# Kernel tuning notes

Measured on AMD Instinct MI355X. Metric: run time of the kernel, lower is better.

The kernel has to match this reference:

```python
import jax, jax.numpy as jnp
import numpy as np

LN_EPS = 1e-5


def setup_inputs() -> dict:
    key = jax.random.key(0)
    ks = jax.random.split(key, 12)
    B, T, U, H, V = 4, 512, 128, 512, 41
    src = jax.random.normal(ks[0], (B, T, H), dtype=jnp.float32)
    tgt = jax.random.normal(ks[1], (B, U, H), dtype=jnp.float32)
    src_len = jax.random.randint(ks[2], (B,), 1, T + 1, dtype=jnp.int32)
    tgt_len = jax.random.randint(ks[3], (B,), 1, U + 1, dtype=jnp.int32)
    s = 1.0 / np.sqrt(H)
    W1 = jax.random.uniform(ks[4], (H, H), jnp.float32, -s, s)
    b1 = jax.random.uniform(ks[5], (H,), jnp.float32, -s, s)
    W2 = jax.random.uniform(ks[6], (H, H), jnp.float32, -s, s)
    b2 = jax.random.uniform(ks[7], (H,), jnp.float32, -s, s)
    ln_g = jnp.ones((H,), jnp.float32)
    ln_b = jnp.zeros((H,), jnp.float32)
    Wl = jax.random.uniform(ks[8], (H, V), jnp.float32, -s, s)
    bl = jax.random.uniform(ks[9], (V,), jnp.float32, -s, s)
    return dict(source_encodings=src, source_lengths=src_len,
                target_encodings=tgt, target_lengths=tgt_len,
                W1=W1, b1=b1, W2=W2, b2=b2, ln_g=ln_g, ln_b=ln_b,
                Wl=Wl, bl=bl)


def _f_target(tgt, W1, b1, W2, b2, ln_g, ln_b):
    h = jax.nn.gelu(tgt @ W1 + b1, approximate=False)  # exact GELU (torch default)
    h = h @ W2 + b2
    mu = jnp.mean(h, axis=-1, keepdims=True)
    var = jnp.var(h, axis=-1, keepdims=True)
    return (h - mu) * jax.lax.rsqrt(var + LN_EPS) * ln_g + ln_b


def reference(source_encodings, source_lengths, target_encodings, target_lengths,
              W1, b1, W2, b2, ln_g, ln_b, Wl, bl):
    tgt = _f_target(target_encodings, W1, b1, W2, b2, ln_g, ln_b)  # [B,U,H]
    # joint broadcast add: [B,T,1,H] + [B,1,U,H] -> [B,T,U,H]
    joint = source_encodings[:, :, None, :] + tgt[:, None, :, :]
    act = jnp.tanh(joint)
    out = act @ Wl + bl  # [B,T,U,V]
    return out, source_lengths, target_lengths
```

## Files before the change

### kernel.cpp

```cpp
#include <hip/hip_runtime.h>
#include <math.h>

#define Bb 4
#define Tt 512
#define Uu 128
#define Hh 512
#define Vv 41

typedef __attribute__((ext_vector_type(8))) short short8;
typedef __attribute__((ext_vector_type(4))) float f32x4;
typedef __attribute__((ext_vector_type(2))) float v2f;

__device__ __forceinline__ unsigned pack_bf16_rne(float hi, float lo) {
    unsigned xh = __float_as_uint(hi); xh += 0x7fffu + ((xh >> 16) & 1u);
    unsigned xl = __float_as_uint(lo); xl += 0x7fffu + ((xl >> 16) & 1u);
    return __builtin_amdgcn_perm(xh, xl, 0x07060302);
}

__device__ __forceinline__ unsigned short bf16_rne(float v) {
    unsigned x = __float_as_uint(v);
    x += 0x7fffu + ((x >> 16) & 1u);
    return (unsigned short)(x >> 16);
}

__device__ __forceinline__ float bf16lo(unsigned u) { return __uint_as_float(u << 16); }
__device__ __forceinline__ float bf16hi(unsigned u) { return __uint_as_float(u & 0xffff0000u); }

__device__ __forceinline__ float tanh_acc(float x) {
    float e = __expf(2.0f * x);
    return 1.0f - 2.0f * __builtin_amdgcn_rcpf(e + 1.0f);
}

__device__ __forceinline__ unsigned mob2(unsigned aw, float ts0, float ts1) {
    v2f tt = {bf16lo(aw), bf16hi(aw)};
    v2f ts = {ts0, ts1};
    v2f nm = ts + tt;
    v2f dn = ts * tt + (v2f){1.f, 1.f};
    v2f g;
    g.x = nm.x * __builtin_amdgcn_rcpf(dn.x);
    g.y = nm.y * __builtin_amdgcn_rcpf(dn.y);
    return __builtin_amdgcn_perm(__float_as_uint(g.y), __float_as_uint(g.x), 0x07060302);
}

__global__ __launch_bounds__(256) void prep_pack(
    const float* __restrict__ W1, const float* __restrict__ W2,
    const float* __restrict__ Wl, const float* __restrict__ tgt,
    unsigned short* __restrict__ Wp1, unsigned short* __restrict__ Wp2,
    unsigned short* __restrict__ Wpl, unsigned short* __restrict__ tgtA,
    const int* __restrict__ sl, const int* __restrict__ tl,
    float* __restrict__ lenDst)
{
    __shared__ __align__(16) char smem[16640];
    const int bid = blockIdx.x, tid = threadIdx.x;

    if (bid >= 136) {
        unsigned short (*At)[520] = (unsigned short (*)[520])smem;
        const int rt = bid - 136;
        const float4* t4 = (const float4*)(tgt + (size_t)rt * 16 * Hh);
        #pragma unroll
        for (int j = 0; j < 8; ++j) {
            int fi = j * 256 + tid;
            int row = fi >> 7, c4 = fi & 127;
            float4 v = t4[fi];
            uint2 pk;
            pk.x = pack_bf16_rne(v.y, v.x);
            pk.y = pack_bf16_rne(v.w, v.z);
            *(uint2*)&At[row][c4 * 4] = pk;
        }
        __syncthreads();
        #pragma unroll
        for (int i = 0; i < 4; ++i) {
            int chunk = i * 256 + tid;
            int ks = chunk >> 6, l = chunk & 63;
            int q = l >> 4, nc = l & 15;
            short8 v = *(const short8*)&At[nc][ks * 32 + q * 8];
            *(short8*)(tgtA + ((size_t)(rt * 16 + ks) * 64 + l) * 8) = v;
        }
        return;
    }

    if (bid == 135 && tid < 2 * Bb)
        lenDst[tid] = (tid < Bb) ? (float)sl[tid] : (float)tl[tid - Bb];

    float (*T)[65] = (float (*)[65])smem;
    const float* Wsrc; unsigned short* Wdst; int k0, n0, isWl;
    if (bid < 64)       { Wsrc = W1; Wdst = Wp1; k0 = (bid >> 3) * 64; n0 = (bid & 7) * 64; isWl = 0; }
    else if (bid < 128) { Wsrc = W2; Wdst = Wp2; k0 = ((bid - 64) >> 3) * 64; n0 = ((bid - 64) & 7) * 64; isWl = 0; }
    else                { Wsrc = Wl; Wdst = Wpl; k0 = (bid - 128) * 64; n0 = 0; isWl = 1; }

    #pragma unroll
    for (int i = 0; i < 16; ++i) {
        int idx = i * 256 + tid;
        int kk = idx >> 6, nn = idx & 63;
        float v;
        if (isWl) v = (nn < Vv) ? Wl[(k0 + kk) * Vv + nn] : 0.0f;
        else      v = Wsrc[(size_t)(k0 + kk) * 512 + n0 + nn];
        T[kk][nn] = v;
    }
    __syncthreads();

    #pragma unroll
    for (int i = 0; i < 2; ++i) {
        int task = i * 256 + tid;
        int nn = task & 63, kg = task >> 6;
        if (isWl && nn >= 48) continue;
        int n = n0 + nn, k = k0 + kg * 8;
        float e[8];
        #pragma unroll
        for (int j = 0; j < 8; ++j) e[j] = T[kg * 8 + j][nn];
        uint4 pk;
        pk.x = pack_bf16_rne(e[1], e[0]);
        pk.y = pack_bf16_rne(e[3], e[2]);
        pk.z = pack_bf16_rne(e[5], e[4]);
        pk.w = pack_bf16_rne(e[7], e[6]);
        int ntg = n >> 4, ncol = n & 15;
        int ks = (k >> 5) & 15, quad = (k >> 3) & 3;
        int lane = quad * 16 + ncol;
        *(uint4*)(Wdst + (size_t)((ntg * 16 + ks) * 64 + lane) * 8) = pk;
    }
}

__global__ __launch_bounds__(128) void gemm_t1(
    const unsigned short* __restrict__ tgtA,
    const unsigned short* __restrict__ Wp1, const float* __restrict__ b1,
    unsigned short* __restrict__ h1A)
{
    __shared__ unsigned short At[16][72];
    const int nb = blockIdx.x, rt = blockIdx.y;
    const int tid = threadIdx.x, lane = tid & 63, w = tid >> 6;
    const int ncol = lane & 15, quad = lane >> 4;
    const int nt0 = nb * 4 + w * 2;

    const unsigned short* ap = tgtA + ((size_t)rt * 1024 + lane) * 8;
    const unsigned short* bp = Wp1 + (size_t)lane * 8;

    f32x4 acc0 = (f32x4){0.f,0.f,0.f,0.f}, acc1 = (f32x4){0.f,0.f,0.f,0.f};
    short8 ac  = *(const short8*)(ap);
    short8 b0c = *(const short8*)(bp + (size_t)nt0 * 8192);
    short8 b1c = *(const short8*)(bp + (size_t)(nt0 + 1) * 8192);

    #pragma unroll
    for (int ks = 0; ks < 16; ++ks) {
        short8 an, b0n, b1n;
        if (ks < 15) {
            an  = *(const short8*)(ap + (ks + 1) * 512);
            b0n = *(const short8*)(bp + (size_t)nt0 * 8192 + (ks + 1) * 512);
            b1n = *(const short8*)(bp + (size_t)(nt0 + 1) * 8192 + (ks + 1) * 512);
        }
        acc0 = __builtin_amdgcn_mfma_f32_16x16x32_bf16(ac, b0c, acc0, 0, 0, 0);
        acc1 = __builtin_amdgcn_mfma_f32_16x16x32_bf16(ac, b1c, acc1, 0, 0, 0);
        ac = an; b0c = b0n; b1c = b1n;
    }

    #pragma unroll
    for (int nt = 0; nt < 2; ++nt) {
        int n = nb * 64 + w * 32 + nt * 16 + ncol;
        float bias = b1[n];
        f32x4 A = nt ? acc1 : acc0;
        #pragma unroll
        for (int r = 0; r < 4; ++r) {
            float v = A[r] + bias;
            float g = 0.5f * v * (1.0f + erff(v * 0.70710678118654752f));
            At[quad * 4 + r][w * 32 + nt * 16 + ncol] = bf16_rne(g);
        }
    }
    __syncthreads();

    {
        int l = lane;
        short8 v = *(const short8*)&At[l & 15][w * 32 + (l >> 4) * 8];
        int ksg = nb * 2 + w;
        *(short8*)(h1A + ((size_t)(rt * 16 + ksg) * 64 + l) * 8) = v;
    }
}

__global__ __launch_bounds__(512) void gemm_t2ln(
    const unsigned short* __restrict__ h1A,
    const unsigned short* __restrict__ Wp2, const float* __restrict__ b2,
    const float* __restrict__ ln_g, const float* __restrict__ ln_b,
    unsigned short* __restrict__ tgtPb)
{
    __shared__ float Ct[16][520];
    const int rt = blockIdx.x;
    const int tid = threadIdx.x, lane = tid & 63, w = tid >> 6;
    const int ncol = lane & 15, quad = lane >> 4;
    const int nt0 = w * 4;

    const unsigned short* ap = h1A + ((size_t)rt * 1024 + lane) * 8;
    const unsigned short* bp = Wp2 + (size_t)lane * 8 + (size_t)nt0 * 8192;

    f32x4 acc[4];
    #pragma unroll
    for (int i = 0; i < 4; ++i) acc[i] = (f32x4){0.f, 0.f, 0.f, 0.f};

    short8 ac = *(const short8*)(ap);
    short8 bc[4];
    #pragma unroll
    for (int i = 0; i < 4; ++i) bc[i] = *(const short8*)(bp + (size_t)i * 8192);

    #pragma unroll
    for (int ks = 0; ks < 16; ++ks) {
        short8 an, bn[4];
        if (ks < 15) {
            an = *(const short8*)(ap + (ks + 1) * 512);
            #pragma unroll
            for (int i = 0; i < 4; ++i)
                bn[i] = *(const short8*)(bp + (size_t)i * 8192 + (ks + 1) * 512);
        }
        #pragma unroll
        for (int i = 0; i < 4; ++i)
            acc[i] = __builtin_amdgcn_mfma_f32_16x16x32_bf16(ac, bc[i], acc[i], 0, 0, 0);
        ac = an;
        #pragma unroll
        for (int i = 0; i < 4; ++i) bc[i] = bn[i];
    }

    #pragma unroll
    for (int nt = 0; nt < 4; ++nt) {
        int n = w * 64 + nt * 16 + ncol;
        float bias = b2[n];
        #pragma unroll
        for (int r = 0; r < 4; ++r)
            Ct[quad * 4 + r][n] = acc[nt][r] + bias;
    }
    __syncthreads();

    #pragma unroll
    for (int rr = 0; rr < 2; ++rr) {
        const int row = w * 2 + rr;
        const float4* cr = (const float4*)&Ct[row][0];
        float4 v0 = cr[lane], v1 = cr[lane + 64];
        float s = v0.x + v0.y + v0.z + v0.w + v1.x + v1.y + v1.z + v1.w;
        float q = v0.x*v0.x + v0.y*v0.y + v0.z*v0.z + v0.w*v0.w
                + v1.x*v1.x + v1.y*v1.y + v1.z*v1.z + v1.w*v1.w;
        #pragma unroll
        for (int off = 32; off > 0; off >>= 1) {
            s += __shfl_xor(s, off, 64);
            q += __shfl_xor(q, off, 64);
        }
        float mu = s * (1.0f / Hh);
        float rs = rsqrtf(q * (1.0f / Hh) - mu * mu + 1e-5f);

        const int r = rt * 16 + row;
        const int bb = r >> 7, u = r & 127;
        #pragma unroll
        for (int j = 0; j < 2; ++j) {
            int k0 = j * 256 + lane * 4;
            float4 v = j ? v1 : v0;
            float4 g4 = ((const float4*)ln_g)[j * 64 + lane];
            float4 b4 = ((const float4*)ln_b)[j * 64 + lane];
            float4 o;
            o.x = tanh_acc((v.x - mu) * rs * g4.x + b4.x);
            o.y = tanh_acc((v.y - mu) * rs * g4.y + b4.y);
            o.z = tanh_acc((v.z - mu) * rs * g4.z + b4.z);
            o.w = tanh_acc((v.w - mu) * rs * g4.w + b4.w);
            uint2 pk;
            pk.x = pack_bf16_rne(o.y, o.x);
            pk.y = pack_bf16_rne(o.w, o.z);
            int chunk = k0 >> 3, half = (k0 >> 2) & 1;
            *(uint2*)(tgtPb + ((size_t)(bb * 64 + chunk) * 128 + u) * 8 + half * 4) = pk;
        }
    }
}

__global__ __launch_bounds__(256) void joint_mfma(
    const float* __restrict__ src, const unsigned short* __restrict__ tgtPb,
    const unsigned short* __restrict__ Wpl, const float* __restrict__ bl,
    float* __restrict__ out)
{
    __shared__ float srcl[2 * Hh];

    const int t0 = blockIdx.x * 2, b = blockIdx.y, uh = blockIdx.z;
    const int tid = threadIdx.x;
    const int lane = tid & 63, wave = tid >> 6;
    const int ncol = lane & 15, quad = lane >> 4;

    {
        const float4* s4 = (const float4*)(src + ((size_t)(b * Tt + t0)) * Hh);
        float4 v = s4[tid];
        v.x = tanh_acc(v.x); v.y = tanh_acc(v.y);
        v.z = tanh_acc(v.z); v.w = tanh_acc(v.w);
        ((float4*)srcl)[tid] = v;
    }

    const int u0 = uh * 64 + (wave & 1) * 32 + ncol;
    const unsigned short* pA = tgtPb + (size_t)b * 65536;
    const unsigned short* bp = Wpl + (size_t)lane * 8;

    uint4 Aa[2], Ac[2];
    short8 Bq[2][3];
    {
        const unsigned short* p0 = pA + ((size_t)(0 * 4 + quad) * 128) * 8;
        Aa[0] = *(const uint4*)(p0 + u0 * 8);
        Ac[0] = *(const uint4*)(p0 + (u0 + 16) * 8);
        Bq[0][0] = *(const short8*)(bp);
        Bq[0][1] = *(const short8*)(bp + 8192);
        Bq[0][2] = *(const short8*)(bp + 16384);
        const unsigned short* p1 = pA + ((size_t)(1 * 4 + quad) * 128) * 8;
        Aa[1] = *(const uint4*)(p1 + u0 * 8);
        Ac[1] = *(const uint4*)(p1 + (u0 + 16) * 8);
        Bq[1][0] = *(const short8*)(bp + 512);
        Bq[1][1] = *(const short8*)(bp + 8192 + 512);
        Bq[1][2] = *(const short8*)(bp + 16384 + 512);
    }

    f32x4 acc[2][3];
    #pragma unroll
    for (int nt = 0; nt < 3; ++nt) {
        int n = nt * 16 + ncol;
        float bv = (n < Vv) ? bl[n] : 0.0f;
        acc[0][nt] = (f32x4){bv, bv, bv, bv};
        acc[1][nt] = (f32x4){bv, bv, bv, bv};
    }

    __syncthreads();
    const float* srow = srcl + (wave >> 1) * Hh;
    float4 sA = *(const float4*)(srow + quad * 8);
    float4 sB = *(const float4*)(srow + quad * 8 + 4);

    #pragma unroll
    for (int ks = 0; ks < 16; ++ks) {
        const int st = ks & 1;
        uint4 a = Aa[st], c = Ac[st];
        short8 B0 = Bq[st][0], B1 = Bq[st][1], B2 = Bq[st][2];

        if (ks + 2 < 16) {
            const unsigned short* pn = pA + ((size_t)((ks + 2) * 4 + quad) * 128) * 8;
            Aa[st] = *(const uint4*)(pn + u0 * 8);
            Ac[st] = *(const uint4*)(pn + (u0 + 16) * 8);
            Bq[st][0] = *(const short8*)(bp + (ks + 2) * 512);
            Bq[st][1] = *(const short8*)(bp + 8192 + (ks + 2) * 512);
            Bq[st][2] = *(const short8*)(bp + 16384 + (ks + 2) * 512);
        }
        float4 nsA, nsB;
        if (ks < 15) {
            nsA = *(const float4*)(srow + (ks + 1) * 32 + quad * 8);
            nsB = *(const float4*)(srow + (ks + 1) * 32 + quad * 8 + 4);
        }

        union { uint4 u; short8 s; } f0, f1;
        f0.u.x = mob2(a.x, sA.x, sA.y);
        f0.u.y = mob2(a.y, sA.z, sA.w);
        f0.u.z = mob2(a.z, sB.x, sB.y);
        f0.u.w = mob2(a.w, sB.z, sB.w);
        f1.u.x = mob2(c.x, sA.x, sA.y);
        f1.u.y = mob2(c.y, sA.z, sA.w);
        f1.u.z = mob2(c.z, sB.x, sB.y);
        f1.u.w = mob2(c.w, sB.z, sB.w);

        acc[0][0] = __builtin_amdgcn_mfma_f32_16x16x32_bf16(f0.s, B0, acc[0][0], 0, 0, 0);
        acc[1][0] = __builtin_amdgcn_mfma_f32_16x16x32_bf16(f1.s, B0, acc[1][0], 0, 0, 0);
        acc[0][1] = __builtin_amdgcn_mfma_f32_16x16x32_bf16(f0.s, B1, acc[0][1], 0, 0, 0);
        acc[1][1] = __builtin_amdgcn_mfma_f32_16x16x32_bf16(f1.s, B1, acc[1][1], 0, 0, 0);
        acc[0][2] = __builtin_amdgcn_mfma_f32_16x16x32_bf16(f0.s, B2, acc[0][2], 0, 0, 0);
        acc[1][2] = __builtin_amdgcn_mfma_f32_16x16x32_bf16(f1.s, B2, acc[1][2], 0, 0, 0);

        sA = nsA; sB = nsB;
    }

    const int t = t0 + (wave >> 1);
    const int ub = uh * 64 + (wave & 1) * 32;
    float* ob = out + ((size_t)(b * Tt + t)) * Uu * Vv;
    #pragma unroll
    for (int mi = 0; mi < 2; ++mi) {
        #pragma unroll
        for (int nt = 0; nt < 3; ++nt) {
            int n = nt * 16 + ncol;
            if (n < Vv) {
                #pragma unroll
                for (int r = 0; r < 4; ++r) {
                    int m = ub + mi * 16 + quad * 4 + r;
                    ob[m * Vv + n] = acc[mi][nt][r];
                }
            }
        }
    }
}

extern "C" void kernel_launch(void* const* d_in, const int* in_sizes, int n_in,
                              void* d_out, int out_size, void* d_ws, size_t ws_size,
                              hipStream_t stream)
{
    const float* src  = (const float*)d_in[0];
    const int*   slen = (const int*)  d_in[1];
    const float* tgt  = (const float*)d_in[2];
    const int*   tlen = (const int*)  d_in[3];
    const float* W1   = (const float*)d_in[4];
    const float* b1   = (const float*)d_in[5];
    const float* W2   = (const float*)d_in[6];
    const float* b2   = (const float*)d_in[7];
    const float* ln_g = (const float*)d_in[8];
    const float* ln_b = (const float*)d_in[9];
    const float* Wl   = (const float*)d_in[10];
    const float* bl   = (const float*)d_in[11];

    float* out = (float*)d_out;
    char* ws = (char*)d_ws;
    unsigned short* tgtPb = (unsigned short*)(ws);
    unsigned short* Wp1   = (unsigned short*)(ws + 524288);
    unsigned short* Wp2   = (unsigned short*)(ws + 1048576);
    unsigned short* Wpl   = (unsigned short*)(ws + 1572864);
    unsigned short* tgtA  = (unsigned short*)(ws + 1638400);
    unsigned short* h1A   = (unsigned short*)(ws + 2162688);

    hipLaunchKernelGGL(prep_pack, dim3(168), dim3(256), 0, stream,
                       W1, W2, Wl, tgt, Wp1, Wp2, Wpl, tgtA,
                       slen, tlen, out + (size_t)Bb * Tt * Uu * Vv);
    hipLaunchKernelGGL(gemm_t1, dim3(8, 32), dim3(128), 0, stream,
                       tgtA, Wp1, b1, h1A);
    hipLaunchKernelGGL(gemm_t2ln, dim3(32), dim3(512), 0, stream,
                       h1A, Wp2, b2, ln_g, ln_b, tgtPb);
    hipLaunchKernelGGL(joint_mfma, dim3(Tt / 2, Bb, 2), dim3(256), 0, stream,
                       src, tgtPb, Wpl, bl, out);
}
```

Before: 142.4 us.

## Stage joint output tile in LDS for coalesced float4 stores, interleave Wl packing

The joint kernel's epilogue now writes the 64x41 accumulator tile for each of two time steps into shared memory, then copies it out with contiguous float4 stores. Previously each lane wrote strided scalar floats to global memory. The Wl packing layout is reordered to be k-major across the three N tiles, so B-fragment loads advance through one pointer with small offsets. This adds about 21KB of LDS and a block-wide barrier, which may lower occupancy, in exchange for fully coalesced writes of the large output.

New measurement: 138.3 us. 1.03x faster.

```diff
diff --git a/kernel.cpp b/kernel.cpp
--- a/kernel.cpp
+++ b/kernel.cpp
@@ -46,7 +46,7 @@
     const float* __restrict__ W1, const float* __restrict__ W2,
     const float* __restrict__ Wl, const float* __restrict__ tgt,
     unsigned short* __restrict__ Wp1, unsigned short* __restrict__ Wp2,
-    unsigned short* __restrict__ Wpl, unsigned short* __restrict__ tgtA,
+    unsigned short* __restrict__ Wpl3, unsigned short* __restrict__ tgtA,
     const int* __restrict__ sl, const int* __restrict__ tl,
     float* __restrict__ lenDst)
 {
@@ -86,7 +86,7 @@
     const float* Wsrc; unsigned short* Wdst; int k0, n0, isWl;
     if (bid < 64)       { Wsrc = W1; Wdst = Wp1; k0 = (bid >> 3) * 64; n0 = (bid & 7) * 64; isWl = 0; }
     else if (bid < 128) { Wsrc = W2; Wdst = Wp2; k0 = ((bid - 64) >> 3) * 64; n0 = ((bid - 64) & 7) * 64; isWl = 0; }
-    else                { Wsrc = Wl; Wdst = Wpl; k0 = (bid - 128) * 64; n0 = 0; isWl = 1; }
+    else                { Wsrc = Wl; Wdst = Wpl3; k0 = (bid - 128) * 64; n0 = 0; isWl = 1; }
 
     #pragma unroll
     for (int i = 0; i < 16; ++i) {
@@ -116,7 +116,9 @@
         int ntg = n >> 4, ncol = n & 15;
         int ks = (k >> 5) & 15, quad = (k >> 3) & 3;
         int lane = quad * 16 + ncol;
-        *(uint4*)(Wdst + (size_t)((ntg * 16 + ks) * 64 + lane) * 8) = pk;
+        size_t slot = isWl ? (size_t)((ks * 3 + ntg) * 64 + lane)
+                           : (size_t)((ntg * 16 + ks) * 64 + lane);
+        *(uint4*)(Wdst + slot * 8) = pk;
     }
 }
 
@@ -265,10 +267,11 @@
 
 __global__ __launch_bounds__(256) void joint_mfma(
     const float* __restrict__ src, const unsigned short* __restrict__ tgtPb,
-    const unsigned short* __restrict__ Wpl, const float* __restrict__ bl,
+    const unsigned short* __restrict__ Wpl3, const float* __restrict__ bl,
     float* __restrict__ out)
 {
     __shared__ float srcl[2 * Hh];
+    __shared__ __align__(16) float tileC[2 * 64 * Vv];
 
     const int t0 = blockIdx.x * 2, b = blockIdx.y, uh = blockIdx.z;
     const int tid = threadIdx.x;
@@ -284,25 +287,23 @@
     }
 
     const int u0 = uh * 64 + (wave & 1) * 32 + ncol;
-    const unsigned short* pA = tgtPb + (size_t)b * 65536;
-    const unsigned short* bp = Wpl + (size_t)lane * 8;
+    const unsigned short* apl = tgtPb + (size_t)b * 65536 + ((size_t)quad * 128 + u0) * 8;
+    const unsigned short* bpl = Wpl3 + (size_t)lane * 8;
 
     uint4 Aa[2], Ac[2];
     short8 Bq[2][3];
-    {
-        const unsigned short* p0 = pA + ((size_t)(0 * 4 + quad) * 128) * 8;
-        Aa[0] = *(const uint4*)(p0 + u0 * 8);
-        Ac[0] = *(const uint4*)(p0 + (u0 + 16) * 8);
-        Bq[0][0] = *(const short8*)(bp);
-        Bq[0][1] = *(const short8*)(bp + 8192);
-        Bq[0][2] = *(const short8*)(bp + 16384);
-        const unsigned short* p1 = pA + ((size_t)(1 * 4 + quad) * 128) * 8;
-        Aa[1] = *(const uint4*)(p1 + u0 * 8);
-        Ac[1] = *(const uint4*)(p1 + (u0 + 16) * 8);
-        Bq[1][0] = *(const short8*)(bp + 512);
-        Bq[1][1] = *(const short8*)(bp + 8192 + 512);
-        Bq[1][2] = *(const short8*)(bp + 16384 + 512);
-    }
+    Aa[0] = *(const uint4*)(apl);
+    Ac[0] = *(const uint4*)(apl + 128);
+    Bq[0][0] = *(const short8*)(bpl);
+    Bq[0][1] = *(const short8*)(bpl + 512);
+    Bq[0][2] = *(const short8*)(bpl + 1024);
+    apl += 4096; bpl += 1536;
+    Aa[1] = *(const uint4*)(apl);
+    Ac[1] = *(const uint4*)(apl + 128);
+    Bq[1][0] = *(const short8*)(bpl);
+    Bq[1][1] = *(const short8*)(bpl + 512);
+    Bq[1][2] = *(const short8*)(bpl + 1024);
+    apl += 4096; bpl += 1536;
 
     f32x4 acc[2][3];
     #pragma unroll
@@ -325,12 +326,12 @@
         short8 B0 = Bq[st][0], B1 = Bq[st][1], B2 = Bq[st][2];
 
         if (ks + 2 < 16) {
-            const unsigned short* pn = pA + ((size_t)((ks + 2) * 4 + quad) * 128) * 8;
-            Aa[st] = *(const uint4*)(pn + u0 * 8);
-            Ac[st] = *(const uint4*)(pn + (u0 + 16) * 8);
-            Bq[st][0] = *(const short8*)(bp + (ks + 2) * 512);
-            Bq[st][1] = *(const short8*)(bp + 8192 + (ks + 2) * 512);
-            Bq[st][2] = *(const short8*)(bp + 16384 + (ks + 2) * 512);
+            Aa[st] = *(const uint4*)(apl);
+            Ac[st] = *(const uint4*)(apl + 128);
+            Bq[st][0] = *(const short8*)(bpl);
+            Bq[st][1] = *(const short8*)(bpl + 512);
+            Bq[st][2] = *(const short8*)(bpl + 1024);
+            apl += 4096; bpl += 1536;
         }
         float4 nsA, nsB;
         if (ks < 15) {
@@ -358,20 +359,34 @@
         sA = nsA; sB = nsB;
     }
 
-    const int t = t0 + (wave >> 1);
-    const int ub = uh * 64 + (wave & 1) * 32;
-    float* ob = out + ((size_t)(b * Tt + t)) * Uu * Vv;
-    #pragma unroll
-    for (int mi = 0; mi < 2; ++mi) {
-        #pragma unroll
-        for (int nt = 0; nt < 3; ++nt) {
-            int n = nt * 16 + ncol;
-            if (n < Vv) {
-                #pragma unroll
-                for (int r = 0; r < 4; ++r) {
-                    int m = ub + mi * 16 + quad * 4 + r;
-                    ob[m * Vv + n] = acc[mi][nt][r];
+    {
+        const int tloc = wave >> 1;
+        const int ubr = (wave & 1) * 32;
+        float* tc = tileC + tloc * (64 * Vv);
+        #pragma unroll
+        for (int mi = 0; mi < 2; ++mi) {
+            #pragma unroll
+            for (int nt = 0; nt < 3; ++nt) {
+                int n = nt * 16 + ncol;
+                if (n < Vv) {
+                    #pragma unroll
+                    for (int r = 0; r < 4; ++r)
+                        tc[(ubr + mi * 16 + quad * 4 + r) * Vv + n] = acc[mi][nt][r];
                 }
+            }
+        }
+    }
+    __syncthreads();
+    {
+        float* ob0 = out + (((size_t)(b * Tt + t0)) * Uu + uh * 64) * Vv;
+        float* ob1 = out + (((size_t)(b * Tt + t0 + 1)) * Uu + uh * 64) * Vv;
+        const float4* tc4 = (const float4*)tileC;
+        #pragma unroll
+        for (int i = 0; i < 3; ++i) {
+            int idx = i * 256 + tid;
+            if (idx < 656) {
+                ((float4*)ob0)[idx] = tc4[idx];
+                ((float4*)ob1)[idx] = tc4[656 + idx];
             }
         }
     }
@@ -399,17 +414,17 @@
     unsigned short* tgtPb = (unsigned short*)(ws);
     unsigned short* Wp1   = (unsigned short*)(ws + 524288);
     unsigned short* Wp2   = (unsigned short*)(ws + 1048576);
-    unsigned short* Wpl   = (unsigned short*)(ws + 1572864);
+    unsigned short* Wpl3  = (unsigned short*)(ws + 1572864);
     unsigned short* tgtA  = (unsigned short*)(ws + 1638400);
     unsigned short* h1A   = (unsigned short*)(ws + 2162688);
 
     hipLaunchKernelGGL(prep_pack, dim3(168), dim3(256), 0, stream,
-                       W1, W2, Wl, tgt, Wp1, Wp2, Wpl, tgtA,
+                       W1, W2, Wl, tgt, Wp1, Wp2, Wpl3, tgtA,
                        slen, tlen, out + (size_t)Bb * Tt * Uu * Vv);
     hipLaunchKernelGGL(gemm_t1, dim3(8, 32), dim3(128), 0, stream,
                        tgtA, Wp1, b1, h1A);
     hipLaunchKernelGGL(gemm_t2ln, dim3(32), dim3(512), 0, stream,
                        h1A, Wp2, b2, ln_g, ln_b, tgtPb);
     hipLaunchKernelGGL(joint_mfma, dim3(Tt / 2, Bb, 2), dim3(256), 0, stream,
-                       src, tgtPb, Wpl, bl, out);
-}
+                       src, tgtPb, Wpl3, bl, out);
+}
```
